# Performance work log

Hardware: AMD Instinct MI355X
Metric: run time of the kernel (lower is better)

## Reference

```python
import jax, jax.numpy as jnp
import numpy as np

B, S, H = 4, 4096, 2048
G, EPG = 4, 16            # num_expert_groups, experts_per_group
E = G * EPG               # num_experts = 64
TOP_K = 2
TOP_GROUPS = min(2, G)


def setup_inputs() -> dict:
    key = jax.random.key(0)
    ks = jax.random.split(key, 6)
    sc = 0.02
    return {
        "x": jax.random.normal(ks[0], (B, S, H), dtype=jnp.float32),
        "Wg": jax.random.normal(ks[1], (H, G), dtype=jnp.float32) * sc,
        "bg": jnp.zeros((G,), jnp.float32),
        "We": jax.random.normal(ks[2], (G, H, EPG), dtype=jnp.float32) * sc,
        "be": jnp.zeros((G, EPG), jnp.float32),
        "Wc1": jax.random.normal(ks[3], (H, H // 4), dtype=jnp.float32) * sc,
        "bc1": jnp.zeros((H // 4,), jnp.float32),
        "Wc2": jax.random.normal(ks[4], (H // 4, 1), dtype=jnp.float32) * sc,
        "bc2": jnp.zeros((1,), jnp.float32),
        "priority": jnp.ones((E,), jnp.float32).at[::EPG].set(1.2),
    }


def reference(x, Wg, bg, We, be, Wc1, bc1, Wc2, bc2, priority):
    N = B * S
    xf = x.reshape(N, H)

    # confidence estimator: Linear -> GELU(exact) -> Linear -> Sigmoid, [N,1]
    conf = jax.nn.sigmoid(jax.nn.gelu(xf @ Wc1 + bc1, approximate=False) @ Wc2 + bc2)

    # group routing (eval mode: no jitter)
    group_probs = jax.nn.softmax(xf @ Wg + bg, axis=-1)          # [N,G]
    tg_probs, tg_idx = jax.lax.top_k(group_probs, TOP_GROUPS)    # [N,2]

    # expert logits for ALL groups at once (grouped GEMM), scaled by priority
    logits = jnp.einsum('nh,ghe->nge', xf, We) + be              # [N,G,EPG]
    logits = logits * priority.reshape(G, EPG)
    probs = jax.nn.softmax(logits, axis=-1)                      # [N,G,EPG]
    c = conf[:, :, None]                                         # [N,1,1]
    probs = probs * c + (1.0 - c) / EPG                          # confidence mixing

    k = min(TOP_K, EPG)
    rows = jnp.arange(N)
    expert_scores = jnp.zeros((N, E), x.dtype)
    # top-2 selected groups are distinct -> global expert indices disjoint -> set is safe
    for g in range(TOP_GROUPS):
        gid = tg_idx[:, g]                                       # [N]
        pg = jnp.take_along_axis(probs, gid[:, None, None], axis=1)[:, 0, :]  # [N,EPG]
        tp, ti = jax.lax.top_k(pg, k)                            # [N,k]
        glob = ti + gid[:, None] * EPG                           # global expert ids
        w = tp * tg_probs[:, g:g + 1]                            # weight by group prob
        expert_scores = expert_scores.at[rows[:, None], glob].set(w)

    expert_scores = expert_scores / (expert_scores.sum(-1, keepdims=True) + 1e-9)

    ts, ti2 = jax.lax.top_k(expert_scores, TOP_K)                # [N,TOP_K]
    dispatch = jnp.zeros_like(expert_scores).at[rows[:, None], ti2].set(ts)
    dispatch = dispatch.reshape(B, S, E)
    combine = dispatch  # torch clones; identical values
    aux_loss = jnp.asarray(0.0, x.dtype)  # eval mode
    return dispatch, combine, aux_loss
```

## Files before the change

kernel.cpp:

```cpp
#include <hip/hip_runtime.h>

#define NTOK 16384
#define HDIM 2048
#define HD4  512
#define NG   4
#define EPG  16
#define NE   64
#define KSPLIT 4

__global__ __launch_bounds__(512) void gemm_conf_kernel(
    const float* __restrict__ x, const float* __restrict__ Wc1,
    const float* __restrict__ bc1, float* __restrict__ h)
{
    __shared__ float Bs[2][16][260];
    __shared__ float As[2][16][68];
    const int tid  = threadIdx.x;
    const int bm   = blockIdx.x;
    const int half = blockIdx.y;
    const int w    = tid >> 6;
    const int lane = tid & 63;
    const int rbase = w * 8;
    const int cb   = lane * 4;

    const bool aStager = (tid < 256);
    const int srow = (tid & 255) >> 2;
    const int skq  = tid & 3;
    const float* xsrc = x + (size_t)(bm * 64 + srow) * HDIM + skq * 4;

    const int kb = tid & 15, sb = tid >> 4;
    const float* wsrc = Wc1 + (size_t)kb * HD4 + half * 256 + sb * 8;

    float acc[8][4];
#pragma unroll
    for (int r = 0; r < 8; ++r)
#pragma unroll
        for (int j = 0; j < 4; ++j) acc[r][j] = 0.0f;

    float4 a0r = make_float4(0.f, 0.f, 0.f, 0.f);
    if (aStager) a0r = *(const float4*)(xsrc);
    float4 b0r = *(const float4*)(wsrc);
    float4 b1r = *(const float4*)(wsrc + 4);

    int cur = 0;
    const int NT = HDIM / 16;

    for (int t = 0; t < NT; ++t) {
        if (aStager) {
            const int kk = skq * 4;
            As[cur][kk + 0][srow] = a0r.x;
            As[cur][kk + 1][srow] = a0r.y;
            As[cur][kk + 2][srow] = a0r.z;
            As[cur][kk + 3][srow] = a0r.w;
        }
        *(float4*)&Bs[cur][kb][sb * 8]     = b0r;
        *(float4*)&Bs[cur][kb][sb * 8 + 4] = b1r;
        if (t + 1 < NT) {
            if (aStager) a0r = *(const float4*)(xsrc + (t + 1) * 16);
            const float* wn = wsrc + (size_t)(t + 1) * 16 * HD4;
            b0r = *(const float4*)(wn);
            b1r = *(const float4*)(wn + 4);
        }
        __syncthreads();

#pragma unroll
        for (int kk = 0; kk < 16; ++kk) {
            float4 av0 = *(const float4*)&As[cur][kk][rbase];
            float4 av1 = *(const float4*)&As[cur][kk][rbase + 4];
            float4 bv  = *(const float4*)&Bs[cur][kk][cb];
            float av[8] = {av0.x, av0.y, av0.z, av0.w,
                           av1.x, av1.y, av1.z, av1.w};
#pragma unroll
            for (int r = 0; r < 8; ++r) {
                acc[r][0] = fmaf(av[r], bv.x, acc[r][0]);
                acc[r][1] = fmaf(av[r], bv.y, acc[r][1]);
                acc[r][2] = fmaf(av[r], bv.z, acc[r][2]);
                acc[r][3] = fmaf(av[r], bv.w, acc[r][3]);
            }
        }
        cur ^= 1;
    }

    const int gcol = half * 256 + cb;
    float4 bq = *(const float4*)(bc1 + gcol);
    float bb[4] = {bq.x, bq.y, bq.z, bq.w};
#pragma unroll
    for (int r = 0; r < 8; ++r) {
        const int row = bm * 64 + rbase + r;
        float o[4];
#pragma unroll
        for (int j = 0; j < 4; ++j) {
            float v = acc[r][j] + bb[j];
            o[j] = 0.5f * v * (1.0f + erff(v * 0.70710678118654752440f));
        }
        *(float4*)(h + (size_t)row * HD4 + gcol) = *(float4*)&o[0];
    }
}

__global__ __launch_bounds__(256) void conf_reduce_kernel(
    const float* __restrict__ h, const float* __restrict__ Wc2,
    const float* __restrict__ bc2, float* __restrict__ conf)
{
    const int wv = threadIdx.x >> 6, lane = threadIdx.x & 63;
    const int n = blockIdx.x * 4 + wv;
    const float* hr = h + (size_t)n * HD4;
    float s = 0.0f;
#pragma unroll
    for (int t = 0; t < 2; ++t) {
        const int j = t * 256 + lane * 4;
        float4 hv = *(const float4*)(hr + j);
        float4 w4 = *(const float4*)(Wc2 + j);
        s = fmaf(hv.x, w4.x, s);
        s = fmaf(hv.y, w4.y, s);
        s = fmaf(hv.z, w4.z, s);
        s = fmaf(hv.w, w4.w, s);
    }
#pragma unroll
    for (int m = 32; m; m >>= 1) s += __shfl_xor(s, m, 64);
    if (lane == 0) {
        float v = s + bc2[0];
        conf[n] = 1.0f / (1.0f + expf(-v));
    }
}

__global__ __launch_bounds__(256) void gemm_experts_kernel(
    const float* __restrict__ x, const float* __restrict__ We,
    float* __restrict__ Elp)
{
    __shared__ float As[16][68];
    __shared__ float Bs[16][68];
    const int tid = threadIdx.x;
    const int bm = blockIdx.x;
    const int ks = blockIdx.y;
    const int tr = tid >> 4, tc = tid & 15;

    float acc[4][4];
#pragma unroll
    for (int i = 0; i < 4; ++i)
#pragma unroll
        for (int j = 0; j < 4; ++j) acc[i][j] = 0.0f;

    const float* xb = x + (size_t)bm * 64 * HDIM;
    const int arow = tid >> 2, ak4 = tid & 3;
    const int bkk = tid >> 4;
    const int bgrp = (tid >> 2) & 3;
    const int be4 = tid & 3;

    const int kbeg = ks * (HDIM / KSPLIT);
    const int kend = kbeg + (HDIM / KSPLIT);
    for (int k0 = kbeg; k0 < kend; k0 += 16) {
        float4 va = *(const float4*)(xb + (size_t)arow * HDIM + k0 + ak4 * 4);
        As[ak4 * 4 + 0][arow] = va.x;
        As[ak4 * 4 + 1][arow] = va.y;
        As[ak4 * 4 + 2][arow] = va.z;
        As[ak4 * 4 + 3][arow] = va.w;
        *(float4*)&Bs[bkk][bgrp * 16 + be4 * 4] =
            *(const float4*)(We + (size_t)bgrp * HDIM * EPG
                             + (size_t)(k0 + bkk) * EPG + be4 * 4);
        __syncthreads();

        float acc_t[4][4];
#pragma unroll
        for (int i = 0; i < 4; ++i)
#pragma unroll
            for (int j = 0; j < 4; ++j) acc_t[i][j] = 0.0f;
#pragma unroll
        for (int k = 0; k < 16; ++k) {
            float av[4], bv[4];
            *(float4*)av = *(const float4*)&As[k][tr * 4];
            *(float4*)bv = *(const float4*)&Bs[k][tc * 4];
#pragma unroll
            for (int i = 0; i < 4; ++i)
#pragma unroll
                for (int j = 0; j < 4; ++j)
                    acc_t[i][j] = fmaf(av[i], bv[j], acc_t[i][j]);
        }
#pragma unroll
        for (int i = 0; i < 4; ++i)
#pragma unroll
            for (int j = 0; j < 4; ++j) acc[i][j] += acc_t[i][j];
        __syncthreads();
    }
#pragma unroll
    for (int i = 0; i < 4; ++i) {
        float o[4] = {acc[i][0], acc[i][1], acc[i][2], acc[i][3]};
        *(float4*)(Elp + ((size_t)ks * NTOK + bm * 64 + tr * 4 + i) * NE + tc * 4)
            = *(float4*)o;
    }
}

__global__ __launch_bounds__(256) void reduce_el_kernel(
    const float* __restrict__ Elp, float* __restrict__ El)
{
    const size_t i = ((size_t)blockIdx.x * 256 + threadIdx.x) * 4;
    float4 a = *(const float4*)(Elp + i);
    float4 b = *(const float4*)(Elp + (size_t)1 * NTOK * NE + i);
    float4 c = *(const float4*)(Elp + (size_t)2 * NTOK * NE + i);
    float4 d = *(const float4*)(Elp + (size_t)3 * NTOK * NE + i);
    float4 r;
    r.x = ((a.x + b.x) + c.x) + d.x;
    r.y = ((a.y + b.y) + c.y) + d.y;
    r.z = ((a.z + b.z) + c.z) + d.z;
    r.w = ((a.w + b.w) + c.w) + d.w;
    *(float4*)(El + i) = r;
}

__global__ __launch_bounds__(256) void gemv_gates_kernel(
    const float* __restrict__ x, const float* __restrict__ Wg,
    float* __restrict__ Gl)
{
    const int wv = threadIdx.x >> 6, lane = threadIdx.x & 63;
    const int n = blockIdx.x * 4 + wv;
    const float* xr = x + (size_t)n * HDIM;
    float a0 = 0, a1 = 0, a2 = 0, a3 = 0;
#pragma unroll
    for (int t = 0; t < 8; ++t) {
        const int k = t * 256 + lane * 4;
        float4 xv = *(const float4*)(xr + k);
        float4 w0 = *(const float4*)(Wg + (size_t)k * NG);
        float4 w1 = *(const float4*)(Wg + (size_t)k * NG + 4);
        float4 w2 = *(const float4*)(Wg + (size_t)k * NG + 8);
        float4 w3 = *(const float4*)(Wg + (size_t)k * NG + 12);
        a0 = fmaf(xv.x, w0.x, a0); a0 = fmaf(xv.y, w1.x, a0);
        a0 = fmaf(xv.z, w2.x, a0); a0 = fmaf(xv.w, w3.x, a0);
        a1 = fmaf(xv.x, w0.y, a1); a1 = fmaf(xv.y, w1.y, a1);
        a1 = fmaf(xv.z, w2.y, a1); a1 = fmaf(xv.w, w3.y, a1);
        a2 = fmaf(xv.x, w0.z, a2); a2 = fmaf(xv.y, w1.z, a2);
        a2 = fmaf(xv.z, w2.z, a2); a2 = fmaf(xv.w, w3.z, a2);
        a3 = fmaf(xv.x, w0.w, a3); a3 = fmaf(xv.y, w1.w, a3);
        a3 = fmaf(xv.z, w2.w, a3); a3 = fmaf(xv.w, w3.w, a3);
    }
#pragma unroll
    for (int m = 32; m; m >>= 1) {
        a0 += __shfl_xor(a0, m, 64);
        a1 += __shfl_xor(a1, m, 64);
        a2 += __shfl_xor(a2, m, 64);
        a3 += __shfl_xor(a3, m, 64);
    }
    if (lane == 0) {
        float4 r; r.x = a0; r.y = a1; r.z = a2; r.w = a3;
        *(float4*)(Gl + (size_t)n * NG) = r;
    }
}

__global__ __launch_bounds__(256) void finalize_kernel(
    const float* __restrict__ El, const float* __restrict__ Gl,
    const float* __restrict__ conf, const float* __restrict__ bgp,
    const float* __restrict__ bep, const float* __restrict__ prp,
    float* __restrict__ out)
{
    const int n = blockIdx.x * 256 + threadIdx.x;

    float gl0 = Gl[(size_t)n * NG + 0] + bgp[0];
    float gl1 = Gl[(size_t)n * NG + 1] + bgp[1];
    float gl2 = Gl[(size_t)n * NG + 2] + bgp[2];
    float gl3 = Gl[(size_t)n * NG + 3] + bgp[3];
    float gm = fmaxf(fmaxf(gl0, gl1), fmaxf(gl2, gl3));
    float e0 = expf(gl0 - gm), e1 = expf(gl1 - gm);
    float e2 = expf(gl2 - gm), e3 = expf(gl3 - gm);
    float gs = e0 + e1 + e2 + e3;
    float gp0 = e0 / gs, gp1 = e1 / gs, gp2 = e2 / gs, gp3 = e3 / gs;

    int g0 = 0; float t0 = gp0;
    if (gp1 > t0) { t0 = gp1; g0 = 1; }
    if (gp2 > t0) { t0 = gp2; g0 = 2; }
    if (gp3 > t0) { t0 = gp3; g0 = 3; }
    int g1 = -1; float t1 = -1.0f;
    if (g0 != 0)              { t1 = gp0; g1 = 0; }
    if (g0 != 1 && gp1 > t1)  { t1 = gp1; g1 = 1; }
    if (g0 != 2 && gp2 > t1)  { t1 = gp2; g1 = 2; }
    if (g0 != 3 && gp3 > t1)  { t1 = gp3; g1 = 3; }

    const float c = conf[n];
    const float uni = (1.0f - c) * (1.0f / 16.0f);

    int ci0, ci1, ci2, ci3;
    float cv0, cv1, cv2, cv3;

    auto proc = [&](int gid, float tp, int& ia, float& va, int& ib, float& vb) {
        const float* base = El + (size_t)n * NE + gid * EPG;
        const float* beb = bep + gid * EPG;
        const float* prb = prp + gid * EPG;
        float lv[16];
#pragma unroll
        for (int e = 0; e < 16; ++e) lv[e] = (base[e] + beb[e]) * prb[e];
        float m = lv[0];
#pragma unroll
        for (int e = 1; e < 16; ++e) m = fmaxf(m, lv[e]);
        float pe[16]; float s = 0.0f;
#pragma unroll
        for (int e = 0; e < 16; ++e) { pe[e] = expf(lv[e] - m); s += pe[e]; }
        const float cs = c / s;
        float bl[16];
#pragma unroll
        for (int e = 0; e < 16; ++e) bl[e] = fmaf(pe[e], cs, uni);
        int i0 = 0; float v0 = bl[0];
#pragma unroll
        for (int e = 1; e < 16; ++e) { if (bl[e] > v0) { v0 = bl[e]; i0 = e; } }
        int i1 = -1; float v1 = -1e30f;
#pragma unroll
        for (int e = 0; e < 16; ++e) {
            if (e != i0 && bl[e] > v1) { v1 = bl[e]; i1 = e; }
        }
        ia = gid * EPG + i0; va = v0 * tp;
        ib = gid * EPG + i1; vb = v1 * tp;
    };
    proc(g0, t0, ci0, cv0, ci1, cv1);
    proc(g1, t1, ci2, cv2, ci3, cv3);

    const float wsum = cv0 + cv1 + cv2 + cv3;
    const float winv = 1.0f / (wsum + 1e-9f);
    const float s0 = cv0 * winv, s1 = cv1 * winv;
    const float s2 = cv2 * winv, s3 = cv3 * winv;

    float bv = s0; int bi = ci0; int bslot = 0;
    if (s1 > bv || (s1 == bv && ci1 < bi)) { bv = s1; bi = ci1; bslot = 1; }
    if (s2 > bv || (s2 == bv && ci2 < bi)) { bv = s2; bi = ci2; bslot = 2; }
    if (s3 > bv || (s3 == bv && ci3 < bi)) { bv = s3; bi = ci3; bslot = 3; }
    float sv = -1.0f; int si = 1 << 30;
    if (bslot != 0 && (s0 > sv || (s0 == sv && ci0 < si))) { sv = s0; si = ci0; }
    if (bslot != 1 && (s1 > sv || (s1 == sv && ci1 < si))) { sv = s1; si = ci1; }
    if (bslot != 2 && (s2 > sv || (s2 == sv && ci2 < si))) { sv = s2; si = ci2; }
    if (bslot != 3 && (s3 > sv || (s3 == sv && ci3 < si))) { sv = s3; si = ci3; }

    float* d0 = out + (size_t)n * NE;
    float* d1 = out + (size_t)NTOK * NE + (size_t)n * NE;
#pragma unroll
    for (int q = 0; q < 16; ++q) {
        const int j = q * 4;
        float4 v;
        v.x = (j + 0 == bi) ? bv : ((j + 0 == si) ? sv : 0.0f);
        v.y = (j + 1 == bi) ? bv : ((j + 1 == si) ? sv : 0.0f);
        v.z = (j + 2 == bi) ? bv : ((j + 2 == si) ? sv : 0.0f);
        v.w = (j + 3 == bi) ? bv : ((j + 3 == si) ? sv : 0.0f);
        *(float4*)(d0 + j) = v;
        *(float4*)(d1 + j) = v;
    }
    if (n == 0) out[(size_t)2 * NTOK * NE] = 0.0f;
}

extern "C" void kernel_launch(void* const* d_in, const int* in_sizes, int n_in,
                              void* d_out, int out_size, void* d_ws, size_t ws_size,
                              hipStream_t stream)
{
    const float* x    = (const float*)d_in[0];
    const float* Wg   = (const float*)d_in[1];
    const float* bg   = (const float*)d_in[2];
    const float* We   = (const float*)d_in[3];
    const float* be   = (const float*)d_in[4];
    const float* Wc1  = (const float*)d_in[5];
    const float* bc1  = (const float*)d_in[6];
    const float* Wc2  = (const float*)d_in[7];
    const float* bc2  = (const float*)d_in[8];
    const float* prio = (const float*)d_in[9];
    float* out = (float*)d_out;

    float* h    = (float*)d_ws;
    float* conf = h + (size_t)NTOK * HD4;
    float* El   = conf + NTOK;
    float* Gl   = El + (size_t)NTOK * NE;
    float* Elp  = h;

    gemm_conf_kernel<<<dim3(NTOK / 64, 2), 512, 0, stream>>>(x, Wc1, bc1, h);
    conf_reduce_kernel<<<NTOK / 4, 256, 0, stream>>>(h, Wc2, bc2, conf);
    gemm_experts_kernel<<<dim3(NTOK / 64, KSPLIT), 256, 0, stream>>>(x, We, Elp);
    reduce_el_kernel<<<(NTOK * NE / 4) / 256, 256, 0, stream>>>(Elp, El);
    gemv_gates_kernel<<<NTOK / 4, 256, 0, stream>>>(x, Wg, Gl);
    finalize_kernel<<<NTOK / 256, 256, 0, stream>>>(El, Gl, conf, bg, be, prio, out);
}
```

Before: 711.4 us.

## Fuse second confidence linear into GEMM epilogue, drop hidden activation buffer

The GELU output of the confidence GEMM is now dotted with Wc2 in registers and wave-reduced in the epilogue. Each of the two column halves writes a partial sum per token, and finalize adds them with bc2 and applies the sigmoid. This removes the 64MB h write and re-read and one kernel launch. The cost is extra shuffle reductions in the GEMM epilogue, and the workspace layout changes so that Elp no longer aliases h.

```diff
diff --git a/kernel.cpp b/kernel.cpp
--- a/kernel.cpp
+++ b/kernel.cpp
@@ -10,7 +10,8 @@
 
 __global__ __launch_bounds__(512) void gemm_conf_kernel(
     const float* __restrict__ x, const float* __restrict__ Wc1,
-    const float* __restrict__ bc1, float* __restrict__ h)
+    const float* __restrict__ bc1, const float* __restrict__ Wc2,
+    float* __restrict__ confp)
 {
     __shared__ float Bs[2][16][260];
     __shared__ float As[2][16][68];
@@ -67,58 +68,47 @@
             float4 av0 = *(const float4*)&As[cur][kk][rbase];
             float4 av1 = *(const float4*)&As[cur][kk][rbase + 4];
             float4 bv  = *(const float4*)&Bs[cur][kk][cb];
-            float av[8] = {av0.x, av0.y, av0.z, av0.w,
-                           av1.x, av1.y, av1.z, av1.w};
-#pragma unroll
-            for (int r = 0; r < 8; ++r) {
-                acc[r][0] = fmaf(av[r], bv.x, acc[r][0]);
-                acc[r][1] = fmaf(av[r], bv.y, acc[r][1]);
-                acc[r][2] = fmaf(av[r], bv.z, acc[r][2]);
-                acc[r][3] = fmaf(av[r], bv.w, acc[r][3]);
-            }
+#define ROWFMA(R, AV)                              \
+            acc[R][0] = fmaf(AV, bv.x, acc[R][0]); \
+            acc[R][1] = fmaf(AV, bv.y, acc[R][1]); \
+            acc[R][2] = fmaf(AV, bv.z, acc[R][2]); \
+            acc[R][3] = fmaf(AV, bv.w, acc[R][3]);
+            ROWFMA(0, av0.x) ROWFMA(1, av0.y) ROWFMA(2, av0.z) ROWFMA(3, av0.w)
+            ROWFMA(4, av1.x) ROWFMA(5, av1.y) ROWFMA(6, av1.z) ROWFMA(7, av1.w)
+#undef ROWFMA
         }
         cur ^= 1;
     }
 
     const int gcol = half * 256 + cb;
     float4 bq = *(const float4*)(bc1 + gcol);
-    float bb[4] = {bq.x, bq.y, bq.z, bq.w};
+    float4 wq = *(const float4*)(Wc2 + gcol);
+    float p[8];
 #pragma unroll
     for (int r = 0; r < 8; ++r) {
-        const int row = bm * 64 + rbase + r;
-        float o[4];
-#pragma unroll
-        for (int j = 0; j < 4; ++j) {
-            float v = acc[r][j] + bb[j];
-            o[j] = 0.5f * v * (1.0f + erff(v * 0.70710678118654752440f));
-        }
-        *(float4*)(h + (size_t)row * HD4 + gcol) = *(float4*)&o[0];
-    }
-}
-
-__global__ __launch_bounds__(256) void conf_reduce_kernel(
-    const float* __restrict__ h, const float* __restrict__ Wc2,
-    const float* __restrict__ bc2, float* __restrict__ conf)
-{
-    const int wv = threadIdx.x >> 6, lane = threadIdx.x & 63;
-    const int n = blockIdx.x * 4 + wv;
-    const float* hr = h + (size_t)n * HD4;
-    float s = 0.0f;
-#pragma unroll
-    for (int t = 0; t < 2; ++t) {
-        const int j = t * 256 + lane * 4;
-        float4 hv = *(const float4*)(hr + j);
-        float4 w4 = *(const float4*)(Wc2 + j);
-        s = fmaf(hv.x, w4.x, s);
-        s = fmaf(hv.y, w4.y, s);
-        s = fmaf(hv.z, w4.z, s);
-        s = fmaf(hv.w, w4.w, s);
-    }
-#pragma unroll
-    for (int m = 32; m; m >>= 1) s += __shfl_xor(s, m, 64);
+        float v0 = acc[r][0] + bq.x;
+        float v1 = acc[r][1] + bq.y;
+        float v2 = acc[r][2] + bq.z;
+        float v3 = acc[r][3] + bq.w;
+        float o0 = 0.5f * v0 * (1.0f + erff(v0 * 0.70710678118654752440f));
+        float o1 = 0.5f * v1 * (1.0f + erff(v1 * 0.70710678118654752440f));
+        float o2 = 0.5f * v2 * (1.0f + erff(v2 * 0.70710678118654752440f));
+        float o3 = 0.5f * v3 * (1.0f + erff(v3 * 0.70710678118654752440f));
+        float s = o0 * wq.x;
+        s = fmaf(o1, wq.y, s);
+        s = fmaf(o2, wq.z, s);
+        s = fmaf(o3, wq.w, s);
+        p[r] = s;
+    }
+#pragma unroll
+    for (int m = 32; m; m >>= 1) {
+#pragma unroll
+        for (int r = 0; r < 8; ++r) p[r] += __shfl_xor(p[r], m, 64);
+    }
     if (lane == 0) {
-        float v = s + bc2[0];
-        conf[n] = 1.0f / (1.0f + expf(-v));
+#pragma unroll
+        for (int r = 0; r < 8; ++r)
+            confp[(size_t)half * NTOK + bm * 64 + rbase + r] = p[r];
     }
 }
 
@@ -244,9 +234,9 @@
 
 __global__ __launch_bounds__(256) void finalize_kernel(
     const float* __restrict__ El, const float* __restrict__ Gl,
-    const float* __restrict__ conf, const float* __restrict__ bgp,
+    const float* __restrict__ confp, const float* __restrict__ bgp,
     const float* __restrict__ bep, const float* __restrict__ prp,
-    float* __restrict__ out)
+    const float* __restrict__ bc2, float* __restrict__ out)
 {
     const int n = blockIdx.x * 256 + threadIdx.x;
 
@@ -270,7 +260,8 @@
     if (g0 != 2 && gp2 > t1)  { t1 = gp2; g1 = 2; }
     if (g0 != 3 && gp3 > t1)  { t1 = gp3; g1 = 3; }
 
-    const float c = conf[n];
+    const float cp = confp[n] + confp[(size_t)NTOK + n] + bc2[0];
+    const float c = 1.0f / (1.0f + expf(-cp));
     const float uni = (1.0f - c) * (1.0f / 16.0f);
 
     int ci0, ci1, ci2, ci3;
@@ -354,16 +345,14 @@
     const float* prio = (const float*)d_in[9];
     float* out = (float*)d_out;
 
-    float* h    = (float*)d_ws;
-    float* conf = h + (size_t)NTOK * HD4;
-    float* El   = conf + NTOK;
-    float* Gl   = El + (size_t)NTOK * NE;
-    float* Elp  = h;
-
-    gemm_conf_kernel<<<dim3(NTOK / 64, 2), 512, 0, stream>>>(x, Wc1, bc1, h);
-    conf_reduce_kernel<<<NTOK / 4, 256, 0, stream>>>(h, Wc2, bc2, conf);
+    float* confp = (float*)d_ws;
+    float* El    = confp + (size_t)2 * NTOK;
+    float* Gl    = El + (size_t)NTOK * NE;
+    float* Elp   = Gl + (size_t)NTOK * NG;
+
+    gemm_conf_kernel<<<dim3(NTOK / 64, 2), 512, 0, stream>>>(x, Wc1, bc1, Wc2, confp);
     gemm_experts_kernel<<<dim3(NTOK / 64, KSPLIT), 256, 0, stream>>>(x, We, Elp);
     reduce_el_kernel<<<(NTOK * NE / 4) / 256, 256, 0, stream>>>(Elp, El);
     gemv_gates_kernel<<<NTOK / 4, 256, 0, stream>>>(x, Wg, Gl);
-    finalize_kernel<<<NTOK / 256, 256, 0, stream>>>(El, Gl, conf, bg, be, prio, out);
-}
+    finalize_kernel<<<NTOK / 256, 256, 0, stream>>>(El, Gl, confp, bg, be, prio, bc2, out);
+}
```

After: 723.8 us. No clear change (+1.7%).
